# Performance work log

Measured on AMD Instinct MI355X. Metric: run time of the kernel, lower is better.

The kernel has to match this reference:

```python
import jax, jax.numpy as jnp
import numpy as np
import math

B, T, D = 2, 2048, 1024
H, HD = 16, 64
E, TOPK, HID = 8, 2, 2048
EPS = 1e-6


def setup_inputs() -> dict:
    key = jax.random.key(0)
    ks = jax.random.split(key, 12)
    s = 0.02
    # RoPE freqs: [T, HD//2, 2] (cos, sin)
    inv = 1.0 / (10000.0 ** (np.arange(0, HD, 2, dtype=np.float32) / HD))
    ang = np.outer(np.arange(T, dtype=np.float32), inv)  # [T, HD//2]
    freqs_cis = jnp.asarray(np.stack([np.cos(ang), np.sin(ang)], axis=-1))
    # causal additive mask [T, T]
    mask = jnp.where(jnp.tril(jnp.ones((T, T), dtype=bool)), 0.0, -jnp.inf).astype(jnp.float32)
    return {
        "x": jax.random.normal(ks[0], (B, T, D), jnp.float32),
        "freqs_cis": freqs_cis,
        "mask": mask,
        "attn_norm_w": jnp.ones((D,), jnp.float32),
        "ffn_norm_w": jnp.ones((D,), jnp.float32),
        "wq": jax.random.normal(ks[1], (D, D), jnp.float32) * s,
        "wk": jax.random.normal(ks[2], (D, D), jnp.float32) * s,
        "wv": jax.random.normal(ks[3], (D, D), jnp.float32) * s,
        "wo": jax.random.normal(ks[4], (D, D), jnp.float32) * s,
        "gate_w": jax.random.normal(ks[5], (D, E), jnp.float32) * s,
        "w1": jax.random.normal(ks[6], (E, D, HID), jnp.float32) * s,
        "w2": jax.random.normal(ks[7], (E, HID, D), jnp.float32) * s,
        "w3": jax.random.normal(ks[8], (E, D, HID), jnp.float32) * s,
    }


def rmsnorm(x, w):
    rms = jax.lax.rsqrt(jnp.mean(x * x, axis=-1, keepdims=True) + EPS)
    return x * rms * w


def rope(q, fc):
    # q: [B, T, H, HD], fc: [T, HD//2, 2]
    qr = q.reshape(*q.shape[:-1], HD // 2, 2)
    cos = fc[None, :, None, :, 0]
    sin = fc[None, :, None, :, 1]
    r0 = qr[..., 0] * cos - qr[..., 1] * sin
    r1 = qr[..., 0] * sin + qr[..., 1] * cos
    return jnp.stack([r0, r1], axis=-1).reshape(q.shape)


def reference(x, freqs_cis, mask, attn_norm_w, ffn_norm_w, wq, wk, wv, wo,
              gate_w, w1, w2, w3):
    # ---- attention sub-block (pre-norm) ----
    h = rmsnorm(x, attn_norm_w)
    q = (h @ wq).reshape(B, T, H, HD)
    k = (h @ wk).reshape(B, T, H, HD)
    v = (h @ wv).reshape(B, T, H, HD)
    q = rope(q, freqs_cis)
    k = rope(k, freqs_cis)
    new_k, new_v = k, v  # kv cache (no prior cache)
    scale = 1.0 / math.sqrt(HD)
    scores = jnp.einsum("bqhd,bkhd->bhqk", q, k) * scale + mask[None, None]
    attn = jax.nn.softmax(scores, axis=-1)
    out = jnp.einsum("bhqk,bkhd->bqhd", attn, v).reshape(B, T, D)
    x = x + out @ wo

    # ---- MoE sub-block (pre-norm) ----
    hf = rmsnorm(x, ffn_norm_w).reshape(-1, D)  # [N, D]
    gate_probs = jax.nn.softmax(hf @ gate_w, axis=-1)  # [N, E]
    topk_vals, topk_idx = jax.lax.top_k(gate_probs, TOPK)
    topk_w = topk_vals / (jnp.sum(topk_vals, axis=-1, keepdims=True) + 1e-8)
    # per-token per-expert combine weight [N, E]
    comb = jnp.sum(topk_w[:, :, None] * jax.nn.one_hot(topk_idx, E), axis=1)
    # dense per-expert SwiGLU (faithful linear combination of expert outputs)
    h1 = jnp.einsum("nd,edh->enh", hf, w1)
    h3 = jnp.einsum("nd,edh->enh", hf, w3)
    y = jnp.einsum("enh,ehd->end", jax.nn.silu(h1) * h3, w2)
    moe_out = jnp.einsum("ne,end->nd", comb, y).reshape(B, T, D)
    x = x + moe_out
    return (x, new_k, new_v)
```

## Files before the change

### kernel.cpp

```cpp
#include <hip/hip_runtime.h>

#define T_SEQ   2048
#define D_MODEL 1024
#define NHEAD   16
#define NEXP    8
#define HID_DIM 2048
#define NTOK    4096
#define MAXBLK  72
#define SLOTS   9216

typedef unsigned short u16;
typedef unsigned int   u32;
typedef __bf16 bf16_t;
typedef bf16_t bf16x8 __attribute__((ext_vector_type(8)));
typedef float  f32x4  __attribute__((ext_vector_type(4)));
typedef float  f32x2  __attribute__((ext_vector_type(2)));
typedef u32    u32x4  __attribute__((ext_vector_type(4)));

typedef __attribute__((address_space(1))) const void* gptr1_t;
typedef __attribute__((address_space(3))) void*       lptr3_t;

__device__ __forceinline__ u16 f2bf_bits(float f) {
  u32 u = __builtin_bit_cast(u32, f);
  u += 0x7FFFu + ((u >> 16) & 1u);
  return (u16)(u >> 16);
}
__device__ __forceinline__ float bf2f(u16 s) {
  return __builtin_bit_cast(float, (u32)s << 16);
}
__device__ __forceinline__ bf16x8 frag_b128(const u16* p) {
  return *reinterpret_cast<const bf16x8*>(p);
}
#define MFMA16(a,b,c) __builtin_amdgcn_mfma_f32_16x16x32_bf16((a),(b),(c),0,0,0)

__device__ __forceinline__ void gload16(const void* g, void* l) {
  __builtin_amdgcn_global_load_lds((gptr1_t)g, (lptr3_t)l, 16, 0, 0);
}

__device__ __forceinline__ void stage128x32(const u16* gbase, size_t ldk, int kt,
                                            u16* lds, int wid, int lane) {
  int rl = lane >> 2, cc = lane & 3;
#pragma unroll
  for (int h = 0; h < 2; ++h) {
    int row = wid*32 + h*16 + rl;
    int chunk = cc ^ ((row >> 1) & 3);
    gload16(gbase + (size_t)row*ldk + kt + chunk*8, lds + (size_t)(wid*32 + h*16)*32);
  }
}
__device__ __forceinline__ bf16x8 fragLDS(const u16* lds, int row, int l4, int l15) {
  int chunk = l4 ^ ((l15 >> 1) & 3);
  return frag_b128(lds + row*32 + chunk*8);
}

template<int SPLIT>
__global__ __launch_bounds__(256) void rmsnorm_kernel(
    const float* __restrict__ x, const float* __restrict__ w,
    u16* __restrict__ hi, u16* __restrict__ lo)
{
  int row = blockIdx.x, tid = threadIdx.x;
  const float* xr = x + (size_t)row * D_MODEL;
  f32x4 v = *reinterpret_cast<const f32x4*>(xr + tid * 4);
  float ss = v[0]*v[0] + v[1]*v[1] + v[2]*v[2] + v[3]*v[3];
#pragma unroll
  for (int off = 32; off >= 1; off >>= 1) ss += __shfl_xor(ss, off);
  __shared__ float part[4];
  if ((tid & 63) == 0) part[tid >> 6] = ss;
  __syncthreads();
  float rms = rsqrtf((part[0]+part[1]+part[2]+part[3]) * (1.0f/D_MODEL) + 1e-6f);
  f32x4 wv = *reinterpret_cast<const f32x4*>(w + tid * 4);
  u32 hw0=0, hw1=0, lw0=0, lw1=0;
#pragma unroll
  for (int j = 0; j < 4; ++j) {
    float f = v[j] * rms * wv[j];
    u16 hb = f2bf_bits(f);
    if (j < 2) hw0 |= (u32)hb << (16*j); else hw1 |= (u32)hb << (16*(j-2));
    if (SPLIT) {
      u16 lb = f2bf_bits(f - bf2f(hb));
      if (j < 2) lw0 |= (u32)lb << (16*j); else lw1 |= (u32)lb << (16*(j-2));
    }
  }
  u32* hp = reinterpret_cast<u32*>(hi + (size_t)row * D_MODEL + tid * 4);
  hp[0] = hw0; hp[1] = hw1;
  if (SPLIT) {
    u32* lp = reinterpret_cast<u32*>(lo + (size_t)row * D_MODEL + tid * 4);
    lp[0] = lw0; lp[1] = lw1;
  }
}

template<int SPLIT>
__global__ __launch_bounds__(256) void transpose_kernel(
    const float* __restrict__ src, u16* __restrict__ dhi, u16* __restrict__ dlo,
    int R, int C)
{
  __shared__ float tile[64][65];
  src += (size_t)blockIdx.z * R * C;
  dhi += (size_t)blockIdx.z * R * C;
  if (SPLIT) dlo += (size_t)blockIdx.z * R * C;
  int r0 = blockIdx.y*64, c0 = blockIdx.x*64;
  int t = threadIdx.x;
  int lr = t>>2, lc4 = (t&3)*16;
#pragma unroll
  for (int i = 0; i < 4; ++i)
    *reinterpret_cast<f32x4*>(&tile[lr][lc4 + i*4]) =
        *reinterpret_cast<const f32x4*>(src + (size_t)(r0+lr)*C + c0 + lc4 + i*4);
  __syncthreads();
#pragma unroll
  for (int h = 0; h < 2; ++h) {
    int oc = h*32 + (t>>3);
    int ok = (t&7)*8;
    union { u16 a[8]; u32x4 v; } hb, lb;
#pragma unroll
    for (int j = 0; j < 8; ++j) {
      float f = tile[ok+j][oc];
      hb.a[j] = f2bf_bits(f);
      if (SPLIT) lb.a[j] = f2bf_bits(f - bf2f(hb.a[j]));
    }
    *reinterpret_cast<u32x4*>(dhi + (size_t)(c0+oc)*R + r0 + ok) = hb.v;
    if (SPLIT)
      *reinterpret_cast<u32x4*>(dlo + (size_t)(c0+oc)*R + r0 + ok) = lb.v;
  }
}

__global__ __launch_bounds__(256) void qkv_gemm_kernel(
    const u16* __restrict__ Ahi, const u16* __restrict__ Alo,
    const u16* __restrict__ Bhi, const u16* __restrict__ Blo,
    const float* __restrict__ freqs,
    u16* __restrict__ qhi, u16* __restrict__ qlo,
    u16* __restrict__ khi, u16* __restrict__ klo,
    u16* __restrict__ vbf, float* __restrict__ kout, float* __restrict__ vout)
{
  const int K = D_MODEL;
  __shared__ __align__(16) u16 AhS[128*32], AlS[128*32], BhS[128*32], BlS[128*32];
  int tid = threadIdx.x, lane = tid & 63, wid = tid >> 6;
  int wm = wid >> 1, wn = wid & 1;
  int l15 = lane & 15, l4 = lane >> 4;
  size_t bm = (size_t)blockIdx.y * 128, bn = (size_t)blockIdx.x * 128;
  const u16* Ah0 = Ahi + bm*K;  const u16* Al0 = Alo + bm*K;
  const u16* Bh0 = Bhi + bn*K;  const u16* Bl0 = Blo + bn*K;
  f32x4 acc[4][4] = {};
  for (int kt = 0; kt < K; kt += 32) {
    __syncthreads();
    stage128x32(Ah0, K, kt, AhS, wid, lane);
    stage128x32(Al0, K, kt, AlS, wid, lane);
    stage128x32(Bh0, K, kt, BhS, wid, lane);
    stage128x32(Bl0, K, kt, BlS, wid, lane);
    __syncthreads();
    bf16x8 ah[4], al[4];
#pragma unroll
    for (int mi = 0; mi < 4; ++mi) {
      int row = wm*64 + mi*16 + l15;
      ah[mi] = fragLDS(AhS, row, l4, l15);
      al[mi] = fragLDS(AlS, row, l4, l15);
    }
#pragma unroll
    for (int ni = 0; ni < 4; ++ni) {
      int row = wn*64 + ni*16 + l15;
      bf16x8 bh = fragLDS(BhS, row, l4, l15);
      bf16x8 bl = fragLDS(BlS, row, l4, l15);
#pragma unroll
      for (int mi = 0; mi < 4; ++mi) {
        acc[mi][ni] = MFMA16(ah[mi], bh, acc[mi][ni]);
        acc[mi][ni] = MFMA16(ah[mi], bl, acc[mi][ni]);
        acc[mi][ni] = MFMA16(al[mi], bh, acc[mi][ni]);
      }
    }
  }
  int mat = (int)(bn >> 10);
  int colbase = (int)(bn & 1023);
#pragma unroll
  for (int mi = 0; mi < 4; ++mi) {
#pragma unroll
    for (int r = 0; r < 4; ++r) {
      int tok = (int)bm + wm*64 + mi*16 + l4*4 + r;
      int t = tok & (T_SEQ - 1);
#pragma unroll
      for (int ni = 0; ni < 4; ++ni) {
        int col = colbase + wn*64 + ni*16 + l15;
        float v = acc[mi][ni][r];
        if (mat == 2) {
          vbf[(size_t)tok*D_MODEL + col] = f2bf_bits(v);
          vout[(size_t)tok*D_MODEL + col] = v;
        } else {
          int d = col & 63, p = d >> 1;
          f32x2 cs = *reinterpret_cast<const f32x2*>(freqs + ((size_t)t*32 + p)*2);
          float partner = __shfl_xor(v, 1);
          float rot = (d & 1) ? (partner*cs[1] + v*cs[0]) : (v*cs[0] - partner*cs[1]);
          u16 hb = f2bf_bits(rot);
          u16 lb = f2bf_bits(rot - bf2f(hb));
          if (mat == 0) {
            qhi[(size_t)tok*D_MODEL + col] = hb;
            qlo[(size_t)tok*D_MODEL + col] = lb;
          } else {
            khi[(size_t)tok*D_MODEL + col] = hb;
            klo[(size_t)tok*D_MODEL + col] = lb;
            kout[(size_t)tok*D_MODEL + col] = rot;
          }
        }
      }
    }
  }
}

__global__ __launch_bounds__(256) void wo_gemm_kernel(
    const u16* __restrict__ A, const u16* __restrict__ Bt,
    const float* __restrict__ resid, float* __restrict__ Cout)
{
  const int K = D_MODEL, N = D_MODEL;
  __shared__ __align__(16) u16 As[128*32], Bs[128*32];
  int tid = threadIdx.x, lane = tid & 63, wid = tid >> 6;
  int wm = wid >> 1, wn = wid & 1;
  int l15 = lane & 15, l4 = lane >> 4;
  size_t bm = (size_t)blockIdx.y * 128, bn = (size_t)blockIdx.x * 128;
  const u16* A0 = A + bm*K;  const u16* B0 = Bt + bn*K;
  f32x4 acc[4][4] = {};
  for (int kt = 0; kt < K; kt += 32) {
    __syncthreads();
    stage128x32(A0, K, kt, As, wid, lane);
    stage128x32(B0, K, kt, Bs, wid, lane);
    __syncthreads();
    bf16x8 a[4];
#pragma unroll
    for (int mi = 0; mi < 4; ++mi)
      a[mi] = fragLDS(As, wm*64 + mi*16 + l15, l4, l15);
#pragma unroll
    for (int ni = 0; ni < 4; ++ni) {
      bf16x8 b = fragLDS(Bs, wn*64 + ni*16 + l15, l4, l15);
#pragma unroll
      for (int mi = 0; mi < 4; ++mi)
        acc[mi][ni] = MFMA16(a[mi], b, acc[mi][ni]);
    }
  }
#pragma unroll
  for (int mi = 0; mi < 4; ++mi)
#pragma unroll
    for (int ni = 0; ni < 4; ++ni)
#pragma unroll
      for (int r = 0; r < 4; ++r) {
        size_t row = bm + wm*64 + mi*16 + l4*4 + r;
        size_t col = bn + wn*64 + ni*16 + l15;
        Cout[row*N + col] = resid[row*N + col] + acc[mi][ni][r];
      }
}

__global__ __launch_bounds__(64) void wg2_kernel(
    const float* __restrict__ wo, const float* __restrict__ ffnw,
    const float* __restrict__ gw, float* __restrict__ wg2)
{
  int d = blockIdx.x, lane = threadIdx.x;
  const float* wr = wo + (size_t)d * D_MODEL;
  float acc[8] = {0,0,0,0,0,0,0,0};
#pragma unroll
  for (int i = 0; i < 4; ++i) {
    int c = lane*4 + i*256;
    f32x4 wv = *reinterpret_cast<const f32x4*>(wr + c);
    f32x4 fv = *reinterpret_cast<const f32x4*>(ffnw + c);
#pragma unroll
    for (int j = 0; j < 4; ++j) {
      float a = wv[j] * fv[j];
      f32x4 g0 = *reinterpret_cast<const f32x4*>(gw + (size_t)(c + j)*NEXP);
      f32x4 g1 = *reinterpret_cast<const f32x4*>(gw + (size_t)(c + j)*NEXP + 4);
      acc[0]+=a*g0[0]; acc[1]+=a*g0[1]; acc[2]+=a*g0[2]; acc[3]+=a*g0[3];
      acc[4]+=a*g1[0]; acc[5]+=a*g1[1]; acc[6]+=a*g1[2]; acc[7]+=a*g1[3];
    }
  }
#pragma unroll
  for (int off = 32; off >= 1; off >>= 1)
#pragma unroll
    for (int e = 0; e < 8; ++e) acc[e] += __shfl_xor(acc[e], off);
  if (lane == 0) {
#pragma unroll
    for (int e = 0; e < 8; ++e) wg2[(size_t)d*NEXP + e] = acc[e];
  }
}

__global__ __launch_bounds__(256) void vg_kernel(
    const float* __restrict__ vf, const float* __restrict__ wg2, float* __restrict__ Vg)
{
  int tok = blockIdx.x * 4 + (threadIdx.x >> 6);
  int lane = threadIdx.x & 63;
  int hh = lane >> 2, part = lane & 3;
  const float* vr = vf + (size_t)tok * D_MODEL + hh*64 + part*16;
  const float* gr = wg2 + (size_t)(hh*64 + part*16) * NEXP;
  float acc[8] = {0,0,0,0,0,0,0,0};
#pragma unroll
  for (int i = 0; i < 4; ++i) {
    f32x4 vv = *reinterpret_cast<const f32x4*>(vr + i*4);
#pragma unroll
    for (int j = 0; j < 4; ++j) {
      float a = vv[j];
      f32x4 g0 = *reinterpret_cast<const f32x4*>(gr + (size_t)(i*4 + j)*NEXP);
      f32x4 g1 = *reinterpret_cast<const f32x4*>(gr + (size_t)(i*4 + j)*NEXP + 4);
      acc[0]+=a*g0[0]; acc[1]+=a*g0[1]; acc[2]+=a*g0[2]; acc[3]+=a*g0[3];
      acc[4]+=a*g1[0]; acc[5]+=a*g1[1]; acc[6]+=a*g1[2]; acc[7]+=a*g1[3];
    }
  }
#pragma unroll
  for (int off = 1; off < 4; off <<= 1)
#pragma unroll
    for (int e = 0; e < 8; ++e) acc[e] += __shfl_xor(acc[e], off);
  if (part == 0) {
#pragma unroll
    for (int e = 0; e < 8; ++e) Vg[((size_t)tok*NHEAD + hh)*NEXP + e] = acc[e];
  }
}

__global__ __launch_bounds__(256) void attn_kernel(
    const u16* __restrict__ Qhi, const u16* __restrict__ Qlo,
    const u16* __restrict__ Khi, const u16* __restrict__ Klo,
    const u16* __restrict__ Vb, const float* __restrict__ Vg,
    u16* __restrict__ Ob, float* __restrict__ raw_ao)
{
  int bh = blockIdx.x, b = bh >> 4, h = bh & 15;
  int qt = blockIdx.y;
  int tid = threadIdx.x, lane = tid & 63, wid = tid >> 6;
  int l15 = lane & 15, l4 = lane >> 4;

  __shared__ __align__(16) u16 VT[64][72];
  __shared__ __align__(16) u16 Pl[4][16][72];
  __shared__ float VgS[64][8];

  size_t qoff = ((size_t)(b*T_SEQ + qt*64 + wid*16)) * D_MODEL + h*64;
  bf16x8 qhiF[2], qloF[2];
#pragma unroll
  for (int s = 0; s < 2; ++s) {
    qhiF[s] = frag_b128(Qhi + qoff + (size_t)l15*D_MODEL + s*32 + l4*8);
    qloF[s] = frag_b128(Qlo + qoff + (size_t)l15*D_MODEL + s*32 + l4*8);
  }
  float m_r[4], l_r[4], racc[4][8];
  f32x4 oacc[4] = {};
#pragma unroll
  for (int r = 0; r < 4; ++r) {
    m_r[r] = -1e30f; l_r[r] = 0.f;
#pragma unroll
    for (int e = 0; e < 8; ++e) racc[r][e] = 0.f;
  }
  int vkey = tid >> 2, vd = (tid & 3) * 16;

  for (int kt = 0; kt <= qt; ++kt) {
    __syncthreads();
    {
      const u16* vsrc = Vb + ((size_t)(b*T_SEQ + kt*64 + vkey))*D_MODEL + h*64 + vd;
      union { u32x4 u[2]; u16 s[16]; } tv;
      tv.u[0] = *reinterpret_cast<const u32x4*>(vsrc);
      tv.u[1] = *reinterpret_cast<const u32x4*>(vsrc + 8);
#pragma unroll
      for (int j = 0; j < 16; ++j) VT[vd + j][vkey] = tv.s[j];
    }
    if (tid < 128) {
      int key = tid >> 1, eh = (tid & 1) * 4;
      const float* gsrc = Vg + ((size_t)(b*T_SEQ + kt*64 + key)*NHEAD + h)*NEXP + eh;
      *reinterpret_cast<f32x4*>(&VgS[key][eh]) = *reinterpret_cast<const f32x4*>(gsrc);
    }
    f32x4 sacc[4] = {};
    const u16* kbaseH = Khi + ((size_t)(b*T_SEQ + kt*64))*D_MODEL + h*64;
    const u16* kbaseL = Klo + ((size_t)(b*T_SEQ + kt*64))*D_MODEL + h*64;
#pragma unroll
    for (int n = 0; n < 4; ++n) {
#pragma unroll
      for (int s = 0; s < 2; ++s) {
        size_t koff = (size_t)(n*16 + l15)*D_MODEL + s*32 + l4*8;
        bf16x8 khiF = frag_b128(kbaseH + koff);
        bf16x8 kloF = frag_b128(kbaseL + koff);
        sacc[n] = MFMA16(qhiF[s], khiF, sacc[n]);
        sacc[n] = MFMA16(qhiF[s], kloF, sacc[n]);
        sacc[n] = MFMA16(qloF[s], khiF, sacc[n]);
      }
    }
    int q0 = qt*64 + wid*16 + l4*4;
    int k00 = kt*64 + l15;
#pragma unroll
    for (int n = 0; n < 4; ++n)
#pragma unroll
      for (int r = 0; r < 4; ++r) {
        float vv = sacc[n][r] * 0.125f;
        if (k00 + n*16 > q0 + r) vv = -1e30f;
        sacc[n][r] = vv;
      }
    float corr[4];
#pragma unroll
    for (int r = 0; r < 4; ++r) {
      float rm = fmaxf(fmaxf(sacc[0][r], sacc[1][r]), fmaxf(sacc[2][r], sacc[3][r]));
#pragma unroll
      for (int off = 1; off < 16; off <<= 1) rm = fmaxf(rm, __shfl_xor(rm, off));
      float mn = fmaxf(m_r[r], rm);
      corr[r] = __expf(m_r[r] - mn);
      m_r[r] = mn;
    }
#pragma unroll
    for (int r = 0; r < 4; ++r) {
      float rs = 0.f;
#pragma unroll
      for (int n = 0; n < 4; ++n) {
        float pp = __expf(sacc[n][r] - m_r[r]);
        sacc[n][r] = pp;
        rs += pp;
      }
#pragma unroll
      for (int off = 1; off < 16; off <<= 1) rs += __shfl_xor(rs, off);
      l_r[r] = l_r[r]*corr[r] + rs;
#pragma unroll
      for (int n2 = 0; n2 < 4; ++n2) oacc[n2][r] *= corr[r];
#pragma unroll
      for (int e = 0; e < 8; ++e) racc[r][e] *= corr[r];
    }
#pragma unroll
    for (int n = 0; n < 4; ++n)
#pragma unroll
      for (int r = 0; r < 4; ++r)
        Pl[wid][l4*4 + r][n*16 + l15] = f2bf_bits(sacc[n][r]);
    __syncthreads();
#pragma unroll
    for (int n = 0; n < 4; ++n) {
      f32x4 g0 = *reinterpret_cast<const f32x4*>(&VgS[n*16 + l15][0]);
      f32x4 g1 = *reinterpret_cast<const f32x4*>(&VgS[n*16 + l15][4]);
#pragma unroll
      for (int r = 0; r < 4; ++r) {
        float pp = sacc[n][r];
        racc[r][0]+=pp*g0[0]; racc[r][1]+=pp*g0[1]; racc[r][2]+=pp*g0[2]; racc[r][3]+=pp*g0[3];
        racc[r][4]+=pp*g1[0]; racc[r][5]+=pp*g1[1]; racc[r][6]+=pp*g1[2]; racc[r][7]+=pp*g1[3];
      }
    }
#pragma unroll
    for (int s = 0; s < 2; ++s) {
      bf16x8 pa = frag_b128(&Pl[wid][l15][s*32 + l4*8]);
#pragma unroll
      for (int n = 0; n < 4; ++n) {
        bf16x8 vb8 = frag_b128(&VT[n*16 + l15][s*32 + l4*8]);
        oacc[n] = MFMA16(pa, vb8, oacc[n]);
      }
    }
  }
  float inv[4];
#pragma unroll
  for (int r = 0; r < 4; ++r) inv[r] = 1.0f / l_r[r];
  size_t obase = ((size_t)(b*T_SEQ + qt*64 + wid*16))*D_MODEL + h*64;
#pragma unroll
  for (int n = 0; n < 4; ++n)
#pragma unroll
    for (int r = 0; r < 4; ++r)
      Ob[obase + (size_t)(l4*4 + r)*D_MODEL + n*16 + l15] = f2bf_bits(oacc[n][r]*inv[r]);
#pragma unroll
  for (int off = 1; off < 16; off <<= 1)
#pragma unroll
    for (int r = 0; r < 4; ++r)
#pragma unroll
      for (int e = 0; e < 8; ++e)
        racc[r][e] += __shfl_xor(racc[r][e], off);
  if (l15 == 0) {
#pragma unroll
    for (int r = 0; r < 4; ++r) {
      size_t tokg = (size_t)(b*T_SEQ) + qt*64 + wid*16 + l4*4 + r;
#pragma unroll
      for (int e = 0; e < 8; ++e)
        raw_ao[(tokg*NHEAD + h)*NEXP + e] = racc[r][e]*inv[r];
    }
  }
}

__global__ void zero_counts_kernel(int* counts) {
  if (threadIdx.x < NEXP) counts[threadIdx.x] = 0;
}

__global__ __launch_bounds__(256) void gate2_kernel(
    const float* __restrict__ x, const float* __restrict__ x2,
    const float* __restrict__ ffnw, const float* __restrict__ gw,
    const float* __restrict__ raw_ao,
    int* __restrict__ gidx, float* __restrict__ gwt, int* __restrict__ counts)
{
  int tok = blockIdx.x * 4 + (threadIdx.x >> 6);
  int lane = threadIdx.x & 63;
  const float* xr = x + (size_t)tok * D_MODEL;
  const float* x2r = x2 + (size_t)tok * D_MODEL;
  float ss = 0.f;
  float lg[8] = {0,0,0,0,0,0,0,0};
#pragma unroll
  for (int i = 0; i < 4; ++i) {
    int d = lane*4 + i*256;
    f32x4 xv = *reinterpret_cast<const f32x4*>(xr + d);
    f32x4 x2v = *reinterpret_cast<const f32x4*>(x2r + d);
    f32x4 wv = *reinterpret_cast<const f32x4*>(ffnw + d);
    ss += x2v[0]*x2v[0] + x2v[1]*x2v[1] + x2v[2]*x2v[2] + x2v[3]*x2v[3];
#pragma unroll
    for (int j = 0; j < 4; ++j) {
      float a = xv[j]*wv[j];
      f32x4 g0 = *reinterpret_cast<const f32x4*>(gw + (size_t)(d + j)*NEXP);
      f32x4 g1 = *reinterpret_cast<const f32x4*>(gw + (size_t)(d + j)*NEXP + 4);
      lg[0]+=a*g0[0]; lg[1]+=a*g0[1]; lg[2]+=a*g0[2]; lg[3]+=a*g0[3];
      lg[4]+=a*g1[0]; lg[5]+=a*g1[1]; lg[6]+=a*g1[2]; lg[7]+=a*g1[3];
    }
  }
#pragma unroll
  for (int off = 1; off < 64; off <<= 1) {
    ss += __shfl_xor(ss, off);
#pragma unroll
    for (int e = 0; e < 8; ++e) lg[e] += __shfl_xor(lg[e], off);
  }
  float ah[8] = {0,0,0,0,0,0,0,0};
  if (lane < 16) {
    const float* ar = raw_ao + ((size_t)tok*NHEAD + lane)*NEXP;
#pragma unroll
    for (int e = 0; e < 8; ++e) ah[e] = ar[e];
  }
#pragma unroll
  for (int off = 1; off < 16; off <<= 1)
#pragma unroll
    for (int e = 0; e < 8; ++e) ah[e] += __shfl_xor(ah[e], off);
  if (lane == 0) {
    float rms = rsqrtf(ss*(1.0f/D_MODEL) + 1e-6f);
    float lo_[8], pp[8];
    float mx = -1e30f;
#pragma unroll
    for (int e = 0; e < 8; ++e) { lo_[e] = (lg[e] + ah[e]) * rms; mx = fmaxf(mx, lo_[e]); }
    float sum = 0.f;
#pragma unroll
    for (int e = 0; e < 8; ++e) { pp[e] = __expf(lo_[e] - mx); sum += pp[e]; }
    float isum = 1.0f/sum;
#pragma unroll
    for (int e = 0; e < 8; ++e) pp[e] *= isum;
    int i0 = 0;
    for (int e = 1; e < 8; ++e) if (pp[e] > pp[i0]) i0 = e;
    int i1 = (i0 == 0) ? 1 : 0;
    for (int e = 0; e < 8; ++e) if (e != i0 && pp[e] > pp[i1]) i1 = e;
    float v0 = pp[i0], v1 = pp[i1];
    float wnorm = 1.0f/(v0 + v1 + 1e-8f);
    gidx[2*tok] = i0; gidx[2*tok+1] = i1;
    gwt[2*tok] = v0*wnorm; gwt[2*tok+1] = v1*wnorm;
    atomicAdd(&counts[i0], 1); atomicAdd(&counts[i1], 1);
  }
}

__global__ __launch_bounds__(256) void scan_kernel(
    const int* __restrict__ counts, int* __restrict__ base, int* __restrict__ fill,
    int* __restrict__ blk_expert, int* __restrict__ perm_token)
{
  if (threadIdx.x == 0) {
    int b = 0, blk = 0;
    for (int e = 0; e < NEXP; ++e) {
      base[e] = b;
      fill[e] = 0;
      int nb = (counts[e] + 127) >> 7;
      for (int i = 0; i < nb; ++i) blk_expert[blk++] = e;
      b += nb << 7;
    }
    for (; blk < MAXBLK; ++blk) blk_expert[blk] = -1;
  }
  for (int i = threadIdx.x; i < SLOTS; i += 256) perm_token[i] = -1;
}

__global__ __launch_bounds__(256) void scatter_kernel(
    const int* __restrict__ gidx, const int* __restrict__ base, int* __restrict__ fill,
    int* __restrict__ perm_token, int* __restrict__ tok_slot)
{
  int t = blockIdx.x * 256 + threadIdx.x;
  if (t >= NTOK) return;
#pragma unroll
  for (int r = 0; r < 2; ++r) {
    int e = gidx[2*t + r];
    int pos = base[e] + atomicAdd(&fill[e], 1);
    perm_token[pos] = t;
    tok_slot[2*t + r] = pos;
  }
}

__global__ __launch_bounds__(256) void moe_gemm1_kernel(
    const u16* __restrict__ Ah, const u16* __restrict__ W1t, const u16* __restrict__ W3t,
    const int* __restrict__ perm_token, const int* __restrict__ blk_expert,
    u16* __restrict__ tbuf)
{
  int mb = blockIdx.y;
  int e = blk_expert[mb];
  if (e < 0) return;
  const int K = D_MODEL;
  __shared__ __align__(16) u16 As[128*32], B1s[128*32], B3s[128*32];
  int tid = threadIdx.x, lane = tid & 63, wid = tid >> 6;
  int wm = wid >> 1, wn = wid & 1;
  int l15 = lane & 15, l4 = lane >> 4;
  size_t bn = (size_t)blockIdx.x * 128;
  const u16* w1e = W1t + (size_t)e * HID_DIM * D_MODEL + bn*K;
  const u16* w3e = W3t + (size_t)e * HID_DIM * D_MODEL + bn*K;
  int rl = lane >> 2, cc = lane & 3;
  int tokA[2];
#pragma unroll
  for (int h = 0; h < 2; ++h) {
    int row = wid*32 + h*16 + rl;
    int t = perm_token[mb*128 + row];
    tokA[h] = t < 0 ? 0 : t;
  }
  f32x4 acc1[4][4] = {}, acc3[4][4] = {};
  for (int kt = 0; kt < K; kt += 32) {
    __syncthreads();
#pragma unroll
    for (int h = 0; h < 2; ++h) {
      int row = wid*32 + h*16 + rl;
      int chunk = cc ^ ((row >> 1) & 3);
      gload16(Ah + (size_t)tokA[h]*K + kt + chunk*8, As + (size_t)(wid*32 + h*16)*32);
    }
    stage128x32(w1e, K, kt, B1s, wid, lane);
    stage128x32(w3e, K, kt, B3s, wid, lane);
    __syncthreads();
    bf16x8 a[4];
#pragma unroll
    for (int mi = 0; mi < 4; ++mi)
      a[mi] = fragLDS(As, wm*64 + mi*16 + l15, l4, l15);
#pragma unroll
    for (int ni = 0; ni < 4; ++ni) {
      int row = wn*64 + ni*16 + l15;
      bf16x8 b1 = fragLDS(B1s, row, l4, l15);
      bf16x8 b3 = fragLDS(B3s, row, l4, l15);
#pragma unroll
      for (int mi = 0; mi < 4; ++mi) {
        acc1[mi][ni] = MFMA16(a[mi], b1, acc1[mi][ni]);
        acc3[mi][ni] = MFMA16(a[mi], b3, acc3[mi][ni]);
      }
    }
  }
#pragma unroll
  for (int mi = 0; mi < 4; ++mi)
#pragma unroll
    for (int ni = 0; ni < 4; ++ni)
#pragma unroll
      for (int r = 0; r < 4; ++r) {
        size_t slot = (size_t)mb*128 + wm*64 + mi*16 + l4*4 + r;
        size_t col = bn + wn*64 + ni*16 + l15;
        float h1 = acc1[mi][ni][r], h3 = acc3[mi][ni][r];
        float sil = h1 / (1.0f + __expf(-h1));
        tbuf[slot*HID_DIM + col] = f2bf_bits(sil * h3);
      }
}

__global__ __launch_bounds__(256) void moe_gemm2_kernel(
    const u16* __restrict__ tbuf, const u16* __restrict__ W2t,
    const int* __restrict__ blk_expert, u16* __restrict__ ybuf)
{
  int mb = blockIdx.y;
  int e = blk_expert[mb];
  if (e < 0) return;
  const int K = HID_DIM, N = D_MODEL;
  __shared__ __align__(16) u16 As[128*32], Bs[128*32];
  int tid = threadIdx.x, lane = tid & 63, wid = tid >> 6;
  int wm = wid >> 1, wn = wid & 1;
  int l15 = lane & 15, l4 = lane >> 4;
  size_t bm = (size_t)mb * 128, bn = (size_t)blockIdx.x * 128;
  const u16* A0 = tbuf + bm*K;
  const u16* B0 = W2t + (size_t)e * D_MODEL * HID_DIM + bn*K;
  f32x4 acc[4][4] = {};
  for (int kt = 0; kt < K; kt += 32) {
    __syncthreads();
    stage128x32(A0, K, kt, As, wid, lane);
    stage128x32(B0, K, kt, Bs, wid, lane);
    __syncthreads();
    bf16x8 a[4];
#pragma unroll
    for (int mi = 0; mi < 4; ++mi)
      a[mi] = fragLDS(As, wm*64 + mi*16 + l15, l4, l15);
#pragma unroll
    for (int ni = 0; ni < 4; ++ni) {
      bf16x8 b = fragLDS(Bs, wn*64 + ni*16 + l15, l4, l15);
#pragma unroll
      for (int mi = 0; mi < 4; ++mi)
        acc[mi][ni] = MFMA16(a[mi], b, acc[mi][ni]);
    }
  }
#pragma unroll
  for (int mi = 0; mi < 4; ++mi)
#pragma unroll
    for (int ni = 0; ni < 4; ++ni)
#pragma unroll
      for (int r = 0; r < 4; ++r) {
        size_t slot = bm + wm*64 + mi*16 + l4*4 + r;
        size_t col = bn + wn*64 + ni*16 + l15;
        ybuf[slot*N + col] = f2bf_bits(acc[mi][ni][r]);
      }
}

__global__ __launch_bounds__(256) void combine_kernel(
    const float* __restrict__ x2, const u16* __restrict__ ybuf,
    const int* __restrict__ tok_slot, const float* __restrict__ gwt,
    float* __restrict__ xout)
{
  int t = blockIdx.x;
  int c = threadIdx.x * 4;
  int s0 = tok_slot[2*t], s1 = tok_slot[2*t+1];
  float w0 = gwt[2*t], w1 = gwt[2*t+1];
  f32x4 xv = *reinterpret_cast<const f32x4*>(x2 + (size_t)t * D_MODEL + c);
  const u16* y0 = ybuf + (size_t)s0 * D_MODEL + c;
  const u16* y1 = ybuf + (size_t)s1 * D_MODEL + c;
  f32x4 o;
#pragma unroll
  for (int j = 0; j < 4; ++j)
    o[j] = xv[j] + w0 * bf2f(y0[j]) + w1 * bf2f(y1[j]);
  *reinterpret_cast<f32x4*>(xout + (size_t)t * D_MODEL + c) = o;
}

extern "C" void kernel_launch(void* const* d_in, const int* in_sizes, int n_in,
                              void* d_out, int out_size, void* d_ws, size_t ws_size,
                              hipStream_t stream)
{
  (void)in_sizes; (void)n_in; (void)out_size; (void)ws_size;
  const float* x     = (const float*)d_in[0];
  const float* freqs = (const float*)d_in[1];
  const float* attnw = (const float*)d_in[3];
  const float* ffnw  = (const float*)d_in[4];
  const float* wq    = (const float*)d_in[5];
  const float* wk    = (const float*)d_in[6];
  const float* wv    = (const float*)d_in[7];
  const float* wo    = (const float*)d_in[8];
  const float* gw    = (const float*)d_in[9];
  const float* w1    = (const float*)d_in[10];
  const float* w2    = (const float*)d_in[11];
  const float* w3    = (const float*)d_in[12];
  float* xout = (float*)d_out;
  float* kout = xout + (size_t)NTOK * D_MODEL;
  float* vout = kout + (size_t)NTOK * D_MODEL;

  const size_t PLANE = (size_t)NTOK * D_MODEL * 2;
  const size_t QKVT  = (size_t)3 * D_MODEL * D_MODEL * 2;
  const size_t TBUFB = (size_t)SLOTS * HID_DIM * 2;
  const size_t WEXP  = (size_t)NEXP * D_MODEL * HID_DIM * 2;
  char* base = (char*)d_ws;
  u16* hhi      = (u16*)(base);
  u16* hlo      = (u16*)(base + PLANE);
  u16* wqkvT_hi = (u16*)(base + 2*PLANE);
  u16* wqkvT_lo = (u16*)(base + 2*PLANE + QKVT);
  u16* woT      = (u16*)(base + 2*PLANE);
  u16* tbuf     = (u16*)(base);
  char* Qb = base + TBUFB;
  u16* qhi = (u16*)(Qb);
  u16* qlo = (u16*)(Qb + PLANE);
  u16* khi = (u16*)(Qb + 2*PLANE);
  u16* klo = (u16*)(Qb + 3*PLANE);
  u16* vbf = (u16*)(Qb + 4*PLANE);
  u16* w1T  = (u16*)(Qb);
  u16* ybuf = (u16*)(Qb);
  char* Sb = Qb + 5*PLANE;
  u16* aobf = (u16*)(Sb);
  u16* w3T  = (u16*)(Sb);
  u16* w2T  = (u16*)(Sb);
  char* Tb = Sb + WEXP;
  u16* hf = (u16*)(Tb);
  float* x2 = (float*)(Tb + PLANE);
  char* p = Tb + PLANE + (size_t)NTOK * D_MODEL * 4;
  float* wg2    = (float*)p;  p += 32768;
  float* Vg     = (float*)p;  p += (size_t)NTOK*NHEAD*NEXP*4;
  float* raw_ao = (float*)p;  p += (size_t)NTOK*NHEAD*NEXP*4;
  int*   gidx   = (int*)p;    p += 32768;
  float* gwt    = (float*)p;  p += 32768;
  int*   tok_slot = (int*)p;  p += 32768;
  int*   perm   = (int*)p;    p += SLOTS*4;
  int*   counts = (int*)p;
  int*   base_  = counts + 8;
  int*   fill_  = counts + 16;
  int*   blk_e  = counts + 24;

  dim3 blk(256);
  rmsnorm_kernel<1><<<NTOK, blk, 0, stream>>>(x, attnw, hhi, hlo);
  wg2_kernel<<<D_MODEL, 64, 0, stream>>>(wo, ffnw, gw, wg2);
  zero_counts_kernel<<<1, 64, 0, stream>>>(counts);
  dim3 tg(16, 16);
  transpose_kernel<1><<<tg, blk, 0, stream>>>(wq, wqkvT_hi,                   wqkvT_lo,                   D_MODEL, D_MODEL);
  transpose_kernel<1><<<tg, blk, 0, stream>>>(wk, wqkvT_hi + (size_t)D_MODEL*D_MODEL,   wqkvT_lo + (size_t)D_MODEL*D_MODEL,   D_MODEL, D_MODEL);
  transpose_kernel<1><<<tg, blk, 0, stream>>>(wv, wqkvT_hi + (size_t)2*D_MODEL*D_MODEL, wqkvT_lo + (size_t)2*D_MODEL*D_MODEL, D_MODEL, D_MODEL);
  dim3 gqkv(24, 32);
  qkv_gemm_kernel<<<gqkv, blk, 0, stream>>>(hhi, hlo, wqkvT_hi, wqkvT_lo, freqs,
                                            qhi, qlo, khi, klo, vbf, kout, vout);
  transpose_kernel<0><<<tg, blk, 0, stream>>>(wo, woT, nullptr, D_MODEL, D_MODEL);
  vg_kernel<<<NTOK/4, blk, 0, stream>>>(vout, wg2, Vg);
  dim3 ga(32, T_SEQ/64);
  attn_kernel<<<ga, blk, 0, stream>>>(qhi, qlo, khi, klo, vbf, Vg, aobf, raw_ao);
  dim3 tw13(HID_DIM/64, D_MODEL/64, NEXP);
  transpose_kernel<0><<<tw13, blk, 0, stream>>>(w1, w1T, nullptr, D_MODEL, HID_DIM);
  dim3 g88(D_MODEL/128, NTOK/128);
  wo_gemm_kernel<<<g88, blk, 0, stream>>>(aobf, woT, x, x2);
  transpose_kernel<0><<<tw13, blk, 0, stream>>>(w3, w3T, nullptr, D_MODEL, HID_DIM);
  rmsnorm_kernel<0><<<NTOK, blk, 0, stream>>>(x2, ffnw, hf, nullptr);
  gate2_kernel<<<NTOK/4, blk, 0, stream>>>(x, x2, ffnw, gw, raw_ao, gidx, gwt, counts);
  scan_kernel<<<1, blk, 0, stream>>>(counts, base_, fill_, blk_e, perm);
  scatter_kernel<<<NTOK/256, blk, 0, stream>>>(gidx, base_, fill_, perm, tok_slot);
  dim3 g1(HID_DIM/128, MAXBLK);
  moe_gemm1_kernel<<<g1, blk, 0, stream>>>(hf, w1T, w3T, perm, blk_e, tbuf);
  dim3 tw2(D_MODEL/64, HID_DIM/64, NEXP);
  transpose_kernel<0><<<tw2, blk, 0, stream>>>(w2, w2T, nullptr, HID_DIM, D_MODEL);
  dim3 g2(D_MODEL/128, MAXBLK);
  moe_gemm2_kernel<<<g2, blk, 0, stream>>>(tbuf, w2T, blk_e, ybuf);
  combine_kernel<<<NTOK, blk, 0, stream>>>(x2, ybuf, tok_slot, gwt, xout);
}
```

Before: 875.2 us.

## Pair causal attention query tiles per block and trim softmax rescaling work

Each attention block now processes two query tiles (pid and 31-pid), which evens out the triangular causal work so all 512 blocks get roughly equal loads. The mask is applied only on the diagonal tile, and the online-softmax rescale is skipped unless the running max rises by more than a threshold. The change also pads and skews the transposed V tile in LDS to reduce bank conflicts, raises wave priority around the MFMA sections, vectorises the expert-gate accumulation, and switches to the hardware bf16 convert. Halving the grid leaves fewer blocks in flight, and the lazy rescale trades a little numerical headroom for fewer exponentials and multiplies.

```diff
diff --git a/kernel.cpp b/kernel.cpp
--- a/kernel.cpp
+++ b/kernel.cpp
@@ -30,6 +30,9 @@
 }
 __device__ __forceinline__ bf16x8 frag_b128(const u16* p) {
   return *reinterpret_cast<const bf16x8*>(p);
+}
+__device__ __forceinline__ u16 cvt_bf16(float f) {
+  return __builtin_bit_cast(u16, (__bf16)f);
 }
 #define MFMA16(a,b,c) __builtin_amdgcn_mfma_f32_16x16x32_bf16((a),(b),(c),0,0,0)
 
@@ -310,149 +313,174 @@
     const u16* __restrict__ Vb, const float* __restrict__ Vg,
     u16* __restrict__ Ob, float* __restrict__ raw_ao)
 {
-  int bh = blockIdx.x, b = bh >> 4, h = bh & 15;
-  int qt = blockIdx.y;
+  int id = blockIdx.x;
+  int bh = id & 31, b = bh >> 4, h = bh & 15;
+  int pid = id >> 5;
   int tid = threadIdx.x, lane = tid & 63, wid = tid >> 6;
   int l15 = lane & 15, l4 = lane >> 4;
 
-  __shared__ __align__(16) u16 VT[64][72];
+  __shared__ __align__(16) u16 VT[64][88];
   __shared__ __align__(16) u16 Pl[4][16][72];
-  __shared__ float VgS[64][8];
-
-  size_t qoff = ((size_t)(b*T_SEQ + qt*64 + wid*16)) * D_MODEL + h*64;
-  bf16x8 qhiF[2], qloF[2];
-#pragma unroll
-  for (int s = 0; s < 2; ++s) {
-    qhiF[s] = frag_b128(Qhi + qoff + (size_t)l15*D_MODEL + s*32 + l4*8);
-    qloF[s] = frag_b128(Qlo + qoff + (size_t)l15*D_MODEL + s*32 + l4*8);
-  }
-  float m_r[4], l_r[4], racc[4][8];
-  f32x4 oacc[4] = {};
-#pragma unroll
-  for (int r = 0; r < 4; ++r) {
-    m_r[r] = -1e30f; l_r[r] = 0.f;
-#pragma unroll
-    for (int e = 0; e < 8; ++e) racc[r][e] = 0.f;
-  }
+  __shared__ float VgS[64][12];
+
   int vkey = tid >> 2, vd = (tid & 3) * 16;
-
-  for (int kt = 0; kt <= qt; ++kt) {
-    __syncthreads();
-    {
-      const u16* vsrc = Vb + ((size_t)(b*T_SEQ + kt*64 + vkey))*D_MODEL + h*64 + vd;
-      union { u32x4 u[2]; u16 s[16]; } tv;
-      tv.u[0] = *reinterpret_cast<const u32x4*>(vsrc);
-      tv.u[1] = *reinterpret_cast<const u32x4*>(vsrc + 8);
-#pragma unroll
-      for (int j = 0; j < 16; ++j) VT[vd + j][vkey] = tv.s[j];
-    }
-    if (tid < 128) {
-      int key = tid >> 1, eh = (tid & 1) * 4;
-      const float* gsrc = Vg + ((size_t)(b*T_SEQ + kt*64 + key)*NHEAD + h)*NEXP + eh;
-      *reinterpret_cast<f32x4*>(&VgS[key][eh]) = *reinterpret_cast<const f32x4*>(gsrc);
-    }
-    f32x4 sacc[4] = {};
-    const u16* kbaseH = Khi + ((size_t)(b*T_SEQ + kt*64))*D_MODEL + h*64;
-    const u16* kbaseL = Klo + ((size_t)(b*T_SEQ + kt*64))*D_MODEL + h*64;
-#pragma unroll
-    for (int n = 0; n < 4; ++n) {
+  int vco = vkey + (vd >> 1);
+
+  for (int ph = 0; ph < 2; ++ph) {
+    int qt = ph ? (31 - pid) : pid;
+    size_t qoff = ((size_t)(b*T_SEQ + qt*64 + wid*16)) * D_MODEL + h*64;
+    bf16x8 qhiF[2], qloF[2];
+#pragma unroll
+    for (int s = 0; s < 2; ++s) {
+      qhiF[s] = frag_b128(Qhi + qoff + (size_t)l15*D_MODEL + s*32 + l4*8);
+      qloF[s] = frag_b128(Qlo + qoff + (size_t)l15*D_MODEL + s*32 + l4*8);
+    }
+    float m_r[4], l_r[4];
+    f32x4 racc4[4][2] = {};
+    f32x4 oacc[4] = {};
+#pragma unroll
+    for (int r = 0; r < 4; ++r) { m_r[r] = -1e30f; l_r[r] = 0.f; }
+
+    for (int kt = 0; kt <= qt; ++kt) {
+      __syncthreads();
+      {
+        const u16* vsrc = Vb + ((size_t)(b*T_SEQ + kt*64 + vkey))*D_MODEL + h*64 + vd;
+        union { u32x4 u[2]; u16 s[16]; } tv;
+        tv.u[0] = *reinterpret_cast<const u32x4*>(vsrc);
+        tv.u[1] = *reinterpret_cast<const u32x4*>(vsrc + 8);
+#pragma unroll
+        for (int j = 0; j < 16; ++j) VT[vd + j][vco] = tv.s[j];
+      }
+      if (tid < 128) {
+        int key = tid >> 1, eh = (tid & 1) * 4;
+        const float* gsrc = Vg + ((size_t)(b*T_SEQ + kt*64 + key)*NHEAD + h)*NEXP + eh;
+        *reinterpret_cast<f32x4*>(&VgS[key][eh]) = *reinterpret_cast<const f32x4*>(gsrc);
+      }
+      f32x4 sacc[4] = {};
+      const u16* kbaseH = Khi + ((size_t)(b*T_SEQ + kt*64))*D_MODEL + h*64;
+      const u16* kbaseL = Klo + ((size_t)(b*T_SEQ + kt*64))*D_MODEL + h*64;
+      __builtin_amdgcn_s_setprio(1);
+#pragma unroll
+      for (int n = 0; n < 4; ++n) {
+#pragma unroll
+        for (int s = 0; s < 2; ++s) {
+          size_t koff = (size_t)(n*16 + l15)*D_MODEL + s*32 + l4*8;
+          bf16x8 khiF = frag_b128(kbaseH + koff);
+          bf16x8 kloF = frag_b128(kbaseL + koff);
+          sacc[n] = MFMA16(qhiF[s], khiF, sacc[n]);
+          sacc[n] = MFMA16(qhiF[s], kloF, sacc[n]);
+          sacc[n] = MFMA16(qloF[s], khiF, sacc[n]);
+        }
+      }
+      __builtin_amdgcn_s_setprio(0);
+#pragma unroll
+      for (int n = 0; n < 4; ++n)
+#pragma unroll
+        for (int r = 0; r < 4; ++r)
+          sacc[n][r] *= 0.125f;
+      if (kt == qt) {
+        int q0 = qt*64 + wid*16 + l4*4;
+        int k00 = kt*64 + l15;
+#pragma unroll
+        for (int n = 0; n < 4; ++n)
+#pragma unroll
+          for (int r = 0; r < 4; ++r)
+            if (k00 + n*16 > q0 + r) sacc[n][r] = -1e30f;
+      }
+      float rm[4];
+#pragma unroll
+      for (int r = 0; r < 4; ++r) {
+        float v = fmaxf(fmaxf(sacc[0][r], sacc[1][r]), fmaxf(sacc[2][r], sacc[3][r]));
+#pragma unroll
+        for (int off = 1; off < 16; off <<= 1) v = fmaxf(v, __shfl_xor(v, off));
+        rm[r] = v;
+      }
+      int needp = (rm[0] > m_r[0]+8.f) | (rm[1] > m_r[1]+8.f) |
+                  (rm[2] > m_r[2]+8.f) | (rm[3] > m_r[3]+8.f);
+      if (__any(needp)) {
+#pragma unroll
+        for (int r = 0; r < 4; ++r) {
+          float mn = fmaxf(m_r[r], rm[r]);
+          float corr = __expf(m_r[r] - mn);
+          m_r[r] = mn;
+          l_r[r] *= corr;
+          racc4[r][0] *= corr; racc4[r][1] *= corr;
+#pragma unroll
+          for (int n = 0; n < 4; ++n) oacc[n][r] *= corr;
+        }
+      }
+#pragma unroll
+      for (int r = 0; r < 4; ++r) {
+        float rs = 0.f;
+#pragma unroll
+        for (int n = 0; n < 4; ++n) {
+          float pp = __expf(sacc[n][r] - m_r[r]);
+          sacc[n][r] = pp;
+          rs += pp;
+        }
+#pragma unroll
+        for (int off = 1; off < 16; off <<= 1) rs += __shfl_xor(rs, off);
+        l_r[r] += rs;
+      }
+#pragma unroll
+      for (int n = 0; n < 4; ++n)
+#pragma unroll
+        for (int r = 0; r < 4; ++r)
+          Pl[wid][l4*4 + r][n*16 + l15] = cvt_bf16(sacc[n][r]);
+      __syncthreads();
+#pragma unroll
+      for (int n = 0; n < 4; ++n) {
+        f32x4 g0 = *reinterpret_cast<const f32x4*>(&VgS[n*16 + l15][0]);
+        f32x4 g1 = *reinterpret_cast<const f32x4*>(&VgS[n*16 + l15][4]);
+#pragma unroll
+        for (int r = 0; r < 4; ++r) {
+          float pp = sacc[n][r];
+          racc4[r][0] += g0 * pp;
+          racc4[r][1] += g1 * pp;
+        }
+      }
+      __builtin_amdgcn_s_setprio(1);
 #pragma unroll
       for (int s = 0; s < 2; ++s) {
-        size_t koff = (size_t)(n*16 + l15)*D_MODEL + s*32 + l4*8;
-        bf16x8 khiF = frag_b128(kbaseH + koff);
-        bf16x8 kloF = frag_b128(kbaseL + koff);
-        sacc[n] = MFMA16(qhiF[s], khiF, sacc[n]);
-        sacc[n] = MFMA16(qhiF[s], kloF, sacc[n]);
-        sacc[n] = MFMA16(qloF[s], khiF, sacc[n]);
-      }
-    }
-    int q0 = qt*64 + wid*16 + l4*4;
-    int k00 = kt*64 + l15;
+        bf16x8 pa = frag_b128(&Pl[wid][l15][s*32 + l4*8]);
+#pragma unroll
+        for (int n = 0; n < 4; ++n) {
+          bf16x8 vb8 = frag_b128(&VT[n*16 + l15][s*32 + l4*8 + 8*n]);
+          oacc[n] = MFMA16(pa, vb8, oacc[n]);
+        }
+      }
+      __builtin_amdgcn_s_setprio(0);
+    }
+    float inv[4];
+#pragma unroll
+    for (int r = 0; r < 4; ++r) inv[r] = 1.0f / l_r[r];
+    size_t obase = ((size_t)(b*T_SEQ + qt*64 + wid*16))*D_MODEL + h*64;
 #pragma unroll
     for (int n = 0; n < 4; ++n)
 #pragma unroll
+      for (int r = 0; r < 4; ++r)
+        Ob[obase + (size_t)(l4*4 + r)*D_MODEL + n*16 + l15] = cvt_bf16(oacc[n][r]*inv[r]);
+    float rv[4][8];
+#pragma unroll
+    for (int r = 0; r < 4; ++r)
+#pragma unroll
+      for (int e = 0; e < 8; ++e)
+        rv[r][e] = (e < 4) ? racc4[r][0][e] : racc4[r][1][e-4];
+#pragma unroll
+    for (int off = 1; off < 16; off <<= 1)
+#pragma unroll
+      for (int r = 0; r < 4; ++r)
+#pragma unroll
+        for (int e = 0; e < 8; ++e)
+          rv[r][e] += __shfl_xor(rv[r][e], off);
+    if (l15 == 0) {
+#pragma unroll
       for (int r = 0; r < 4; ++r) {
-        float vv = sacc[n][r] * 0.125f;
-        if (k00 + n*16 > q0 + r) vv = -1e30f;
-        sacc[n][r] = vv;
-      }
-    float corr[4];
-#pragma unroll
-    for (int r = 0; r < 4; ++r) {
-      float rm = fmaxf(fmaxf(sacc[0][r], sacc[1][r]), fmaxf(sacc[2][r], sacc[3][r]));
-#pragma unroll
-      for (int off = 1; off < 16; off <<= 1) rm = fmaxf(rm, __shfl_xor(rm, off));
-      float mn = fmaxf(m_r[r], rm);
-      corr[r] = __expf(m_r[r] - mn);
-      m_r[r] = mn;
-    }
-#pragma unroll
-    for (int r = 0; r < 4; ++r) {
-      float rs = 0.f;
-#pragma unroll
-      for (int n = 0; n < 4; ++n) {
-        float pp = __expf(sacc[n][r] - m_r[r]);
-        sacc[n][r] = pp;
-        rs += pp;
-      }
-#pragma unroll
-      for (int off = 1; off < 16; off <<= 1) rs += __shfl_xor(rs, off);
-      l_r[r] = l_r[r]*corr[r] + rs;
-#pragma unroll
-      for (int n2 = 0; n2 < 4; ++n2) oacc[n2][r] *= corr[r];
-#pragma unroll
-      for (int e = 0; e < 8; ++e) racc[r][e] *= corr[r];
-    }
-#pragma unroll
-    for (int n = 0; n < 4; ++n)
-#pragma unroll
-      for (int r = 0; r < 4; ++r)
-        Pl[wid][l4*4 + r][n*16 + l15] = f2bf_bits(sacc[n][r]);
-    __syncthreads();
-#pragma unroll
-    for (int n = 0; n < 4; ++n) {
-      f32x4 g0 = *reinterpret_cast<const f32x4*>(&VgS[n*16 + l15][0]);
-      f32x4 g1 = *reinterpret_cast<const f32x4*>(&VgS[n*16 + l15][4]);
-#pragma unroll
-      for (int r = 0; r < 4; ++r) {
-        float pp = sacc[n][r];
-        racc[r][0]+=pp*g0[0]; racc[r][1]+=pp*g0[1]; racc[r][2]+=pp*g0[2]; racc[r][3]+=pp*g0[3];
-        racc[r][4]+=pp*g1[0]; racc[r][5]+=pp*g1[1]; racc[r][6]+=pp*g1[2]; racc[r][7]+=pp*g1[3];
-      }
-    }
-#pragma unroll
-    for (int s = 0; s < 2; ++s) {
-      bf16x8 pa = frag_b128(&Pl[wid][l15][s*32 + l4*8]);
-#pragma unroll
-      for (int n = 0; n < 4; ++n) {
-        bf16x8 vb8 = frag_b128(&VT[n*16 + l15][s*32 + l4*8]);
-        oacc[n] = MFMA16(pa, vb8, oacc[n]);
-      }
-    }
-  }
-  float inv[4];
-#pragma unroll
-  for (int r = 0; r < 4; ++r) inv[r] = 1.0f / l_r[r];
-  size_t obase = ((size_t)(b*T_SEQ + qt*64 + wid*16))*D_MODEL + h*64;
-#pragma unroll
-  for (int n = 0; n < 4; ++n)
-#pragma unroll
-    for (int r = 0; r < 4; ++r)
-      Ob[obase + (size_t)(l4*4 + r)*D_MODEL + n*16 + l15] = f2bf_bits(oacc[n][r]*inv[r]);
-#pragma unroll
-  for (int off = 1; off < 16; off <<= 1)
-#pragma unroll
-    for (int r = 0; r < 4; ++r)
-#pragma unroll
-      for (int e = 0; e < 8; ++e)
-        racc[r][e] += __shfl_xor(racc[r][e], off);
-  if (l15 == 0) {
-#pragma unroll
-    for (int r = 0; r < 4; ++r) {
-      size_t tokg = (size_t)(b*T_SEQ) + qt*64 + wid*16 + l4*4 + r;
-#pragma unroll
-      for (int e = 0; e < 8; ++e)
-        raw_ao[(tokg*NHEAD + h)*NEXP + e] = racc[r][e]*inv[r];
+        size_t tokg = (size_t)(b*T_SEQ) + qt*64 + wid*16 + l4*4 + r;
+#pragma unroll
+        for (int e = 0; e < 8; ++e)
+          raw_ao[(tokg*NHEAD + h)*NEXP + e] = rv[r][e]*inv[r];
+      }
     }
   }
 }
@@ -765,8 +793,7 @@
                                             qhi, qlo, khi, klo, vbf, kout, vout);
   transpose_kernel<0><<<tg, blk, 0, stream>>>(wo, woT, nullptr, D_MODEL, D_MODEL);
   vg_kernel<<<NTOK/4, blk, 0, stream>>>(vout, wg2, Vg);
-  dim3 ga(32, T_SEQ/64);
-  attn_kernel<<<ga, blk, 0, stream>>>(qhi, qlo, khi, klo, vbf, Vg, aobf, raw_ao);
+  attn_kernel<<<dim3(512), blk, 0, stream>>>(qhi, qlo, khi, klo, vbf, Vg, aobf, raw_ao);
   dim3 tw13(HID_DIM/64, D_MODEL/64, NEXP);
   transpose_kernel<0><<<tw13, blk, 0, stream>>>(w1, w1T, nullptr, D_MODEL, HID_DIM);
   dim3 g88(D_MODEL/128, NTOK/128);
```

Measured after the change: 859.1 us. About the same (-1.8%).
